# Kernel optimization log

Measured on AMD Instinct MI355X. Metric: run time of the kernel, lower is better.

The kernel has to match this reference:

```python
import jax, jax.numpy as jnp
import numpy as np

MAX_KL = 11  # max kernel length among {7,9,11}

def setup_inputs() -> dict:
    key = jax.random.key(0)
    T, K, C = 2048, 10000, 10  # input_length, n_kernels, nr_classes
    rng = np.random.default_rng(0)
    # --- ROCKET random kernels (faithful to build_kernels) ---
    Ls = rng.choice(np.array([7, 9, 11]), size=K)                  # kernel lengths
    w = rng.normal(size=(K, MAX_KL)).astype(np.float32)
    tapmask = np.arange(MAX_KL)[None, :] < Ls[:, None]
    w = w * tapmask
    w = (w - tapmask * (w.sum(1, keepdims=True) / Ls[:, None])).astype(np.float32)  # mean-centered
    b = (1.0 - 2.0 * rng.random(K)).astype(np.float32)             # bias in (-1, 1]
    A = np.log2((T - 1) / (Ls - 1.0))
    dil = np.floor(2.0 ** (rng.random(K) * A)).astype(np.int32)    # dilation
    pad = (rng.random(K) <= 0.5).astype(np.int32)                  # padding 0 or 1
    # --- input series and classifier params ---
    x = jax.random.normal(key, (1, 1, T), dtype=jnp.float32)
    k1, _ = jax.random.split(jax.random.fold_in(key, 1))
    Wc = (jax.random.normal(k1, (2 * K, C), dtype=jnp.float32) * 0.01).astype(jnp.float32)
    bc = jnp.zeros((C,), dtype=jnp.float32)
    return {
        "x": x,
        "w": jnp.asarray(w), "b": jnp.asarray(b),
        "dil": jnp.asarray(dil), "pad": jnp.asarray(pad), "Ls": jnp.asarray(Ls, jnp.int32),
        "Wc": Wc, "bc": bc,
    }


def reference(x, w, b, dil, pad, Ls, Wc, bc):
    # x: [1,1,T]; w: [K,11] (zero-padded taps); b,dil,pad,Ls: [K]; Wc: [2K,C]; bc: [C]
    T = x.shape[-1]
    K = w.shape[0]
    xp = jnp.pad(x[0, 0], (1, 1))                  # [T+2] padded signal (covers padding=1)
    S = T + 2                                      # max possible output length
    s = jnp.arange(S)                              # output positions
    start = (1 - pad)[:, None]                     # [K,1] offset into padded signal
    # out[i,s] = b_i + sum_j w[i,j] * xp[start_i + s + dil_i*j]
    out = jnp.broadcast_to(b[:, None], (K, S))
    for j in range(MAX_KL):                        # fixed small tap loop
        idx = jnp.clip(start + s[None, :] + dil[:, None] * j, 0, T + 1)  # [K,S]
        out = out + w[:, j:j + 1] * xp[idx]
    out_len = T + 2 * pad - dil * (Ls - 1)         # [K] true conv output lengths
    valid = s[None, :] < out_len[:, None]          # [K,S]
    ppv = jnp.sum(jnp.where(valid & (out > 0), 1.0, 0.0), axis=1) / out_len.astype(out.dtype)
    mx = jnp.max(jnp.where(valid, out, -jnp.inf), axis=1)
    feats = jnp.concatenate([ppv, mx])             # [2K] (ppv block then max block)
    return jax.nn.softmax(feats @ Wc + bc, axis=-1)
```

## Files before the change

### kernel.cpp

```cpp
#include <hip/hip_runtime.h>
#include <math.h>

#define T_LEN 2048
#define KNUM 10000
#define MAXKL 11
#define XP_PAD 3456
#define NB2 40
#define CHUNK2 500
#define NCLS 10

__global__ __launch_bounds__(256) void rocket_feats_kernel(
    const float* __restrict__ x, const float* __restrict__ w,
    const float* __restrict__ b, const int* __restrict__ dil,
    const int* __restrict__ pad, const int* __restrict__ Ls,
    float* __restrict__ feats)
{
    __shared__ float xp[XP_PAD];
    __shared__ float wmx[4];
    __shared__ int   wcnt[4];

    const int tid = threadIdx.x;
    const int k   = blockIdx.x;

    for (int i = tid; i < XP_PAD; i += 256) {
        const int src = i - 1;
        float v = 0.0f;
        if (src >= 0 && src < T_LEN) v = x[src];
        xp[i] = v;
    }

    float wr[MAXKL];
#pragma unroll
    for (int j = 0; j < MAXKL; ++j) wr[j] = w[k * MAXKL + j];
    const float bias = b[k];
    const int d  = dil[k];
    const int p  = pad[k];
    const int L  = Ls[k];
    const int out_len = T_LEN + 2 * p - d * (L - 1);
    const int s0 = 1 - p;

    __syncthreads();

    int   cnt = 0;
    float mx  = -INFINITY;
    for (int s = tid; s < out_len; s += 256) {
        const int base = s0 + s;
        float acc = bias;
#pragma unroll
        for (int j = 0; j < MAXKL; ++j)
            acc = fmaf(wr[j], xp[base + j * d], acc);
        cnt += (acc > 0.0f) ? 1 : 0;
        mx = fmaxf(mx, acc);
    }

#pragma unroll
    for (int off = 32; off > 0; off >>= 1) {
        cnt += __shfl_down(cnt, off);
        mx = fmaxf(mx, __shfl_down(mx, off));
    }
    const int wave = tid >> 6;
    if ((tid & 63) == 0) { wmx[wave] = mx; wcnt[wave] = cnt; }
    __syncthreads();
    if (tid == 0) {
        float m = wmx[0];
        int   c = wcnt[0];
#pragma unroll
        for (int i = 1; i < 4; ++i) { m = fmaxf(m, wmx[i]); c += wcnt[i]; }
        feats[k]        = (float)c / (float)out_len;
        feats[KNUM + k] = m;
    }
}

__global__ __launch_bounds__(256) void rocket_logits_kernel(
    const float* __restrict__ feats, const float* __restrict__ Wc,
    float* __restrict__ partials)
{
    float acc[NCLS];
#pragma unroll
    for (int c = 0; c < NCLS; ++c) acc[c] = 0.0f;

    const int fbeg = blockIdx.x * CHUNK2;
    const int fend = fbeg + CHUNK2;
    for (int f = fbeg + threadIdx.x; f < fend; f += 256) {
        const float v = feats[f];
        const float* __restrict__ wrow = Wc + (size_t)f * NCLS;
#pragma unroll
        for (int c = 0; c < NCLS; ++c)
            acc[c] = fmaf(v, wrow[c], acc[c]);
    }

#pragma unroll
    for (int c = 0; c < NCLS; ++c) {
#pragma unroll
        for (int off = 32; off > 0; off >>= 1)
            acc[c] += __shfl_down(acc[c], off);
    }
    __shared__ float lds[4][NCLS];
    const int wave = threadIdx.x >> 6;
    if ((threadIdx.x & 63) == 0) {
#pragma unroll
        for (int c = 0; c < NCLS; ++c) lds[wave][c] = acc[c];
    }
    __syncthreads();
    if (threadIdx.x == 0) {
#pragma unroll
        for (int c = 0; c < NCLS; ++c)
            partials[blockIdx.x * NCLS + c] =
                lds[0][c] + lds[1][c] + lds[2][c] + lds[3][c];
    }
}

__global__ __launch_bounds__(64) void rocket_softmax_kernel(
    const float* __restrict__ partials, const float* __restrict__ bc,
    float* __restrict__ out)
{
    __shared__ float lg[NCLS];
    const int t = threadIdx.x;
    if (t < NCLS) {
        float s = bc[t];
        for (int i = 0; i < NB2; ++i) s += partials[i * NCLS + t];
        lg[t] = s;
    }
    __syncthreads();
    if (t == 0) {
        float m = lg[0];
#pragma unroll
        for (int i = 1; i < NCLS; ++i) m = fmaxf(m, lg[i]);
        float e[NCLS];
        float se = 0.0f;
#pragma unroll
        for (int i = 0; i < NCLS; ++i) { e[i] = expf(lg[i] - m); se += e[i]; }
        const float inv = 1.0f / se;
#pragma unroll
        for (int i = 0; i < NCLS; ++i) out[i] = e[i] * inv;
    }
}

extern "C" void kernel_launch(void* const* d_in, const int* in_sizes, int n_in,
                              void* d_out, int out_size, void* d_ws, size_t ws_size,
                              hipStream_t stream) {
    const float* x   = (const float*)d_in[0];
    const float* w   = (const float*)d_in[1];
    const float* b   = (const float*)d_in[2];
    const int*   dil = (const int*)d_in[3];
    const int*   pad = (const int*)d_in[4];
    const int*   Ls  = (const int*)d_in[5];
    const float* Wc  = (const float*)d_in[6];
    const float* bc  = (const float*)d_in[7];
    float* out = (float*)d_out;

    float* feats    = (float*)d_ws;
    float* partials = feats + 2 * KNUM;

    rocket_feats_kernel<<<KNUM, 256, 0, stream>>>(x, w, b, dil, pad, Ls, feats);
    rocket_logits_kernel<<<NB2, 256, 0, stream>>>(feats, Wc, partials);
    rocket_softmax_kernel<<<1, 64, 0, stream>>>(partials, bc, out);
}
```

Measured before the change: 99.59 us.

## Process eight kernels per block with vectorized staging and tap-length specialization

Each block now handles eight ROCKET kernels instead of one, so the staged input signal in shared memory is reused across kernels rather than reloaded 10000 times. The staging uses float4 loads into a tighter padded buffer. The conv loop is templated on kernel length to skip zero taps, and each thread computes two adjacent outputs. This cuts grid size and redundant global loads, at the cost of fewer blocks for parallelism and serialized per-kernel reductions with a barrier each.

After: 101.4 us. About the same (+1.9%).

```diff
diff --git a/kernel.cpp b/kernel.cpp
--- a/kernel.cpp
+++ b/kernel.cpp
@@ -4,10 +4,38 @@
 #define T_LEN 2048
 #define KNUM 10000
 #define MAXKL 11
-#define XP_PAD 3456
+#define BPK 8
+#define NBLK (KNUM / BPK)
+#define XOFF 3
+#define XP_SZ 2064
 #define NB2 40
 #define CHUNK2 500
 #define NCLS 10
+
+template<int L>
+__device__ __forceinline__ void conv_loop(const float* __restrict__ XP, int tid,
+    int out_len, int s0, int d, const float* __restrict__ wr, float bias,
+    int& cnt, float& mx)
+{
+    for (int s2 = tid * 2; s2 < out_len; s2 += 512) {
+        const int base = XOFF + s0 + s2;
+        float a0 = bias, a1 = bias;
+#pragma unroll
+        for (int j = 0; j < L; ++j) {
+            const float* p = XP + base + j * d;
+            const float p0 = p[0];
+            const float p1 = p[1];
+            a0 = fmaf(wr[j], p0, a0);
+            a1 = fmaf(wr[j], p1, a1);
+        }
+        cnt += (a0 > 0.0f) ? 1 : 0;
+        mx = fmaxf(mx, a0);
+        if (s2 + 1 < out_len) {
+            cnt += (a1 > 0.0f) ? 1 : 0;
+            mx = fmaxf(mx, a1);
+        }
+    }
+}
 
 __global__ __launch_bounds__(256) void rocket_feats_kernel(
     const float* __restrict__ x, const float* __restrict__ w,
@@ -15,59 +43,57 @@
     const int* __restrict__ pad, const int* __restrict__ Ls,
     float* __restrict__ feats)
 {
-    __shared__ float xp[XP_PAD];
-    __shared__ float wmx[4];
-    __shared__ int   wcnt[4];
+    __shared__ float XP[XP_SZ];
+    __shared__ float rmx[BPK][4];
+    __shared__ int   rcnt[BPK][4];
 
     const int tid = threadIdx.x;
-    const int k   = blockIdx.x;
 
-    for (int i = tid; i < XP_PAD; i += 256) {
-        const int src = i - 1;
-        float v = 0.0f;
-        if (src >= 0 && src < T_LEN) v = x[src];
-        xp[i] = v;
+    {
+        const float4* x4 = (const float4*)x;
+        float4* XP4 = (float4*)XP;
+#pragma unroll
+        for (int it = 0; it < T_LEN / 4 / 256; ++it)
+            XP4[1 + it * 256 + tid] = x4[it * 256 + tid];
+        if (tid < 4) XP[tid] = 0.0f;
+        else if (tid < 8) XP[2048 + tid] = 0.0f;
     }
-
-    float wr[MAXKL];
-#pragma unroll
-    for (int j = 0; j < MAXKL; ++j) wr[j] = w[k * MAXKL + j];
-    const float bias = b[k];
-    const int d  = dil[k];
-    const int p  = pad[k];
-    const int L  = Ls[k];
-    const int out_len = T_LEN + 2 * p - d * (L - 1);
-    const int s0 = 1 - p;
-
     __syncthreads();
 
-    int   cnt = 0;
-    float mx  = -INFINITY;
-    for (int s = tid; s < out_len; s += 256) {
-        const int base = s0 + s;
-        float acc = bias;
+    const int k0 = blockIdx.x * BPK;
+    for (int kk = 0; kk < BPK; ++kk) {
+        const int k = k0 + kk;
+        float wr[MAXKL];
 #pragma unroll
-        for (int j = 0; j < MAXKL; ++j)
-            acc = fmaf(wr[j], xp[base + j * d], acc);
-        cnt += (acc > 0.0f) ? 1 : 0;
-        mx = fmaxf(mx, acc);
-    }
+        for (int j = 0; j < MAXKL; ++j) wr[j] = w[k * MAXKL + j];
+        const float bias = b[k];
+        const int d = dil[k];
+        const int p = pad[k];
+        const int L = Ls[k];
+        const int out_len = T_LEN + 2 * p - d * (L - 1);
+        const int s0 = 1 - p;
+
+        int cnt = 0;
+        float mx = -INFINITY;
+        if (L == 7)       conv_loop<7>(XP, tid, out_len, s0, d, wr, bias, cnt, mx);
+        else if (L == 9)  conv_loop<9>(XP, tid, out_len, s0, d, wr, bias, cnt, mx);
+        else              conv_loop<11>(XP, tid, out_len, s0, d, wr, bias, cnt, mx);
 
 #pragma unroll
-    for (int off = 32; off > 0; off >>= 1) {
-        cnt += __shfl_down(cnt, off);
-        mx = fmaxf(mx, __shfl_down(mx, off));
-    }
-    const int wave = tid >> 6;
-    if ((tid & 63) == 0) { wmx[wave] = mx; wcnt[wave] = cnt; }
-    __syncthreads();
-    if (tid == 0) {
-        float m = wmx[0];
-        int   c = wcnt[0];
-#pragma unroll
-        for (int i = 1; i < 4; ++i) { m = fmaxf(m, wmx[i]); c += wcnt[i]; }
-        feats[k]        = (float)c / (float)out_len;
-        feats[KNUM + k] = m;
+        for (int off = 32; off > 0; off >>= 1) {
+            cnt += __shfl_down(cnt, off);
+            mx = fmaxf(mx, __shfl_down(mx, off));
+        }
+        const int wv = tid >> 6;
+        if ((tid & 63) == 0) { rmx[kk][wv] = mx; rcnt[kk][wv] = cnt; }
+        __syncthreads();
+        if (tid == 0) {
+            const float m = fmaxf(fmaxf(rmx[kk][0], rmx[kk][1]),
+                                  fmaxf(rmx[kk][2], rmx[kk][3]));
+            const int c = rcnt[kk][0] + rcnt[kk][1] + rcnt[kk][2] + rcnt[kk][3];
+            feats[k]        = (float)c / (float)out_len;
+            feats[KNUM + k] = m;
+        }
     }
 }
 
@@ -152,7 +178,7 @@
     float* feats    = (float*)d_ws;
     float* partials = feats + 2 * KNUM;
 
-    rocket_feats_kernel<<<KNUM, 256, 0, stream>>>(x, w, b, dil, pad, Ls, feats);
+    rocket_feats_kernel<<<NBLK, 256, 0, stream>>>(x, w, b, dil, pad, Ls, feats);
     rocket_logits_kernel<<<NB2, 256, 0, stream>>>(feats, Wc, partials);
     rocket_softmax_kernel<<<1, 64, 0, stream>>>(partials, bc, out);
 }
```
